# Performance work log

Hardware: AMD Instinct MI355X
Metric: run time of the kernel (lower is better)

## Reference

```python
import jax, jax.numpy as jnp
import numpy as np

T, IN_DIM, H1, H2 = 64, 84, 128, 84
BATCH = 8192


def _glorot(key, shape, fan):
    bound = 1.0 / np.sqrt(fan)
    return jax.random.uniform(key, shape, jnp.float32, -bound, bound)


def setup_inputs() -> dict:
    key = jax.random.key(0)
    ks = jax.random.split(key, 13)
    x = jax.random.normal(ks[0], (BATCH, T, IN_DIM, 1), jnp.float32)
    # rnn1 layer 0: 84 -> 128
    w_ih_l0 = _glorot(ks[1], (H1, IN_DIM), H1)
    w_hh_l0 = _glorot(ks[2], (H1, H1), H1)
    b_ih_l0 = _glorot(ks[3], (H1,), H1)
    b_hh_l0 = _glorot(ks[4], (H1,), H1)
    # rnn1 layer 1: 128 -> 128
    w_ih_l1 = _glorot(ks[5], (H1, H1), H1)
    w_hh_l1 = _glorot(ks[6], (H1, H1), H1)
    b_ih_l1 = _glorot(ks[7], (H1,), H1)
    b_hh_l1 = _glorot(ks[8], (H1,), H1)
    # rnn2: 128 -> 84
    w_ih_l2 = _glorot(ks[9], (H2, H1), H2)
    w_hh_l2 = _glorot(ks[10], (H2, H2), H2)
    b_ih_l2 = _glorot(ks[11], (H2,), H2)
    b_hh_l2 = _glorot(ks[12], (H2,), H2)
    return {
        "x": x,
        "w_ih_l0": w_ih_l0, "w_hh_l0": w_hh_l0, "b_ih_l0": b_ih_l0, "b_hh_l0": b_hh_l0,
        "w_ih_l1": w_ih_l1, "w_hh_l1": w_hh_l1, "b_ih_l1": b_ih_l1, "b_hh_l1": b_hh_l1,
        "w_ih_l2": w_ih_l2, "w_hh_l2": w_hh_l2, "b_ih_l2": b_ih_l2, "b_hh_l2": b_hh_l2,
    }


def _elman_layer(x, w_ih, w_hh, b_ih, b_hh):
    # x: (B, T, I) -> (B, T, H); h_t = tanh(x_t W_ih^T + b_ih + h_{t-1} W_hh^T + b_hh)
    # Precompute the input projection for all timesteps as one big GEMM.
    xp = jnp.einsum('bti,hi->bth', x, w_ih) + (b_ih + b_hh)  # (B, T, H)
    h0 = jnp.zeros((x.shape[0], w_hh.shape[0]), x.dtype)

    def step(h, xp_t):
        h = jnp.tanh(xp_t + h @ w_hh.T)
        return h, h

    _, ys = jax.lax.scan(step, h0, jnp.swapaxes(xp, 0, 1))  # (T, B, H)
    return jnp.swapaxes(ys, 0, 1)


def reference(x,
              w_ih_l0, w_hh_l0, b_ih_l0, b_hh_l0,
              w_ih_l1, w_hh_l1, b_ih_l1, b_hh_l1,
              w_ih_l2, w_hh_l2, b_ih_l2, b_hh_l2):
    x_ = jnp.squeeze(x, -1)                                   # (B, 64, 84)
    h = _elman_layer(x_, w_ih_l0, w_hh_l0, b_ih_l0, b_hh_l0)  # (B, 64, 128)
    h = _elman_layer(h, w_ih_l1, w_hh_l1, b_ih_l1, b_hh_l1)   # (B, 64, 128)
    h = _elman_layer(h, w_ih_l2, w_hh_l2, b_ih_l2, b_hh_l2)   # (B, 64, 84)
    return h[..., None]                                       # (B, 64, 84, 1)
```

## Files before the change

### kernel.cpp

```cpp
#include <hip/hip_runtime.h>


typedef __bf16 bf16x8 __attribute__((ext_vector_type(8)));
typedef float  f32x4  __attribute__((ext_vector_type(4)));
typedef float  f32x16 __attribute__((ext_vector_type(16)));
typedef unsigned short u16;
typedef unsigned int   u32;
typedef u16 u16x8 __attribute__((ext_vector_type(8)));
typedef u16 u16x4 __attribute__((ext_vector_type(4)));

#define MFMA32(a, b, c) __builtin_amdgcn_mfma_f32_32x32x16_bf16((a), (b), (c), 0, 0, 0)

__device__ __forceinline__ float bf2f(u16 v) {
    return __builtin_bit_cast(float, (u32)v << 16);
}
__device__ __forceinline__ u16 f2bf(float f) {
    u32 u = __builtin_bit_cast(u32, f);
    u = u + 0x7fffu + ((u >> 16) & 1u);
    return (u16)(u >> 16);
}
__device__ __forceinline__ float tanh_fast(float x) {
    float xc = fminf(fmaxf(x, -12.f), 12.f);
    float e  = __expf(2.f * xc);
    return (e - 1.f) * __builtin_amdgcn_rcpf(e + 1.f);
}
__device__ __forceinline__ bf16x8 ld_lds8(const u16* p) {
    return __builtin_bit_cast(bf16x8, *(const u16x8*)p);
}
__device__ __forceinline__ int aswz(int row, int off) {
    return row * 128 + (off ^ ((row & 7) << 3));
}
__device__ __forceinline__ void store4_hl(u16* ph, u16* pl, f32x4 v) {
    u16x4 hi, lo;
#pragma unroll
    for (int j = 0; j < 4; j++) {
        u16 h = f2bf(v[j]);
        hi[j] = h;
        lo[j] = f2bf(v[j] - bf2f(h));
    }
    *(u16x4*)ph = hi;
    *(u16x4*)pl = lo;
}

struct fragp { bf16x8 h, l; };

__device__ __forceinline__ fragp load_wfrag_hl(const float* W, int Hr, int Kr,
                                               int n, int kbase) {
    u16x8 uh = {0,0,0,0,0,0,0,0}, ul = {0,0,0,0,0,0,0,0};
    if (n < Hr) {
#pragma unroll
        for (int j = 0; j < 8; j++) {
            int k = kbase + j;
            if (k < Kr) {
                float w = W[n * Kr + k];
                u16 hi = f2bf(w);
                uh[j] = hi;
                ul[j] = f2bf(w - bf2f(hi));
            }
        }
    }
    fragp r;
    r.h = __builtin_bit_cast(bf16x8, uh);
    r.l = __builtin_bit_cast(bf16x8, ul);
    return r;
}

__device__ __forceinline__ f32x16 mm3t(const fragp& w, bf16x8 ah, bf16x8 al, f32x16 c) {
    c = MFMA32(w.h, ah, c);
    c = MFMA32(w.l, ah, c);
    c = MFMA32(w.h, al, c);
    return c;
}

#define STG_ISSUE(trr)                                                   \
    {                                                                    \
        const int tofs = (trr) * 84;                                     \
        _Pragma("unroll")                                                \
        for (int j = 0; j < 5; j++) xs[j] = xg[goff[j] + tofs];          \
        if (tid_s < 128) xs[5] = xg[goff[5] + tofs];                     \
    }
#define STG_WRITE(PNv)                                                   \
    {                                                                    \
        u16* bh = (&xbh[0][0][0]) + (PNv) * 3072;                        \
        u16* bl = (&xbl[0][0][0]) + (PNv) * 3072;                        \
        _Pragma("unroll")                                                \
        for (int j = 0; j < 5; j++) {                                    \
            u16 hi = f2bf(xs[j]);                                        \
            bh[lofs[j]] = hi;                                            \
            bl[lofs[j]] = f2bf(xs[j] - bf2f(hi));                        \
        }                                                                \
        if (tid_s < 128) {                                               \
            u16 hi = f2bf(xs[5]);                                        \
            bh[lofs[5]] = hi;                                            \
            bl[lofs[5]] = f2bf(xs[5] - bf2f(hi));                        \
        }                                                                \
    }

__global__ __launch_bounds__(768, 3)
void rnn_fused(const float* __restrict__ x,
               const float* __restrict__ wih0, const float* __restrict__ whh0,
               const float* __restrict__ bih0, const float* __restrict__ bhh0,
               const float* __restrict__ wih1, const float* __restrict__ whh1,
               const float* __restrict__ bih1, const float* __restrict__ bhh1,
               const float* __restrict__ wih2, const float* __restrict__ whh2,
               const float* __restrict__ bih2, const float* __restrict__ bhh2,
               float* __restrict__ out)
{
    __shared__ __align__(16) u16 h0h[2][4096], h0l[2][4096];
    __shared__ __align__(16) u16 h1h[2][4096], h1l[2][4096];
    __shared__ __align__(16) u16 h2h[2][4096], h2l[2][4096];
    __shared__ __align__(16) u16 xbh[2][32][96], xbl[2][32][96];
    __shared__ float biasF[3][128];

    const int tid  = threadIdx.x;
    const int wv   = tid >> 6;
    const int lane = tid & 63;
    const int mrow = lane & 31;
    const int q2   = lane >> 5;
    const int kq   = q2 * 8;
    const int q4   = q2 * 4;
    const int b0   = blockIdx.x * 32;
    const float* xg = x + (long)b0 * 5376;

    { u16* z = &h0h[0][0]; for (int i = tid; i < 4096; i += 768) z[i] = 0; }
    { u16* z = &h0l[0][0]; for (int i = tid; i < 4096; i += 768) z[i] = 0; }
    { u16* z = &h1h[1][0]; for (int i = tid; i < 4096; i += 768) z[i] = 0; }
    { u16* z = &h1l[1][0]; for (int i = tid; i < 4096; i += 768) z[i] = 0; }
    { u16* z = &h2h[0][0]; for (int i = tid; i < 4096; i += 768) z[i] = 0; }
    { u16* z = &h2l[0][0]; for (int i = tid; i < 4096; i += 768) z[i] = 0; }
    for (int i = tid; i < 32 * 12 * 2; i += 768) {
        int par = i / (32 * 12), rem = i - par * 32 * 12;
        int row = rem / 12, col = 84 + rem - row * 12;
        xbh[par][row][col] = 0; xbl[par][row][col] = 0;
    }
    for (int i = tid; i < 2688; i += 768) {
        int row = i / 84, col = i - row * 84;
        float v = xg[(long)row * 5376 + col];
        u16 hi = f2bf(v);
        xbh[0][row][col] = hi;
        xbl[0][row][col] = f2bf(v - bf2f(hi));
    }
    for (int i = tid; i < 384; i += 768) {
        int l = i >> 7, n = i & 127;
        float v = 0.f;
        if (l == 0)      v = bih0[n] + bhh0[n];
        else if (l == 1) v = bih1[n] + bhh1[n];
        else if (n < 84) v = bih2[n] + bhh2[n];
        biasF[l][n] = v;
    }
    __syncthreads();

    if (wv < 4) {
        const int nb = wv * 32;
        fragp fih0[6], fhh0[8];
#pragma unroll
        for (int c = 0; c < 6; c++)
            fih0[c] = load_wfrag_hl(wih0, 128, 84, nb + mrow, c * 16 + kq);
#pragma unroll
        for (int c = 0; c < 8; c++)
            fhh0[c] = load_wfrag_hl(whh0, 128, 128, nb + mrow, c * 16 + kq);
        const int tid_s = wv * 64 + lane;
        int goff[6], lofs[6];
#pragma unroll
        for (int j = 0; j < 6; j++) {
            int i = tid_s + j * 512, row = i / 84, cc = i - row * 84;
            goff[j] = row * 5376 + cc; lofs[j] = row * 96 + cc;
        }
        float xs[6];

        for (int rr = 0; rr < 66; ++rr) {
            const int P = rr & 1, PN = P ^ 1;
            if (rr <= 62) STG_ISSUE(rr + 1);
            if (rr <= 63) {
                f32x16 acc;
#pragma unroll
                for (int g = 0; g < 4; g++) {
                    f32x4 v = *(const f32x4*)&biasF[0][nb + g * 8 + q4];
                    acc[4*g+0] = v[0]; acc[4*g+1] = v[1];
                    acc[4*g+2] = v[2]; acc[4*g+3] = v[3];
                }
                __builtin_amdgcn_s_setprio(1);
#pragma unroll
                for (int c = 0; c < 6; c++) {
                    const int off = c * 16 + kq;
                    acc = mm3t(fih0[c], ld_lds8(&xbh[P][mrow][off]),
                                        ld_lds8(&xbl[P][mrow][off]), acc);
                }
#pragma unroll
                for (int c = 0; c < 8; c++) {
                    const int idx = aswz(mrow, c * 16 + kq);
                    acc = mm3t(fhh0[c], ld_lds8(&h0h[P][idx]), ld_lds8(&h0l[P][idx]), acc);
                }
                __builtin_amdgcn_s_setprio(0);
#pragma unroll
                for (int g = 0; g < 4; g++) {
                    const int col = nb + g * 8 + q4;
                    f32x4 v;
                    v[0] = tanh_fast(acc[4*g+0]); v[1] = tanh_fast(acc[4*g+1]);
                    v[2] = tanh_fast(acc[4*g+2]); v[3] = tanh_fast(acc[4*g+3]);
                    const int idx = mrow * 128 + (col ^ ((mrow & 7) << 3));
                    store4_hl(&h0h[PN][idx], &h0l[PN][idx], v);
                }
            }
            if (rr <= 62) STG_WRITE(PN);
            __syncthreads();
        }
    } else if (wv < 8) {
        const int nb = (wv - 4) * 32;
        fragp fih1[8], fhh1[8];
#pragma unroll
        for (int c = 0; c < 8; c++) {
            fih1[c] = load_wfrag_hl(wih1, 128, 128, nb + mrow, c * 16 + kq);
            fhh1[c] = load_wfrag_hl(whh1, 128, 128, nb + mrow, c * 16 + kq);
        }
        for (int rr = 0; rr < 66; ++rr) {
            const int P = rr & 1, PN = P ^ 1;
            if (rr >= 1 && rr <= 64) {
                f32x16 acc;
#pragma unroll
                for (int g = 0; g < 4; g++) {
                    f32x4 v = *(const f32x4*)&biasF[1][nb + g * 8 + q4];
                    acc[4*g+0] = v[0]; acc[4*g+1] = v[1];
                    acc[4*g+2] = v[2]; acc[4*g+3] = v[3];
                }
                __builtin_amdgcn_s_setprio(1);
#pragma unroll
                for (int c = 0; c < 8; c++) {
                    const int idx = aswz(mrow, c * 16 + kq);
                    acc = mm3t(fih1[c], ld_lds8(&h0h[P][idx]), ld_lds8(&h0l[P][idx]), acc);
                }
#pragma unroll
                for (int c = 0; c < 8; c++) {
                    const int idx = aswz(mrow, c * 16 + kq);
                    acc = mm3t(fhh1[c], ld_lds8(&h1h[P][idx]), ld_lds8(&h1l[P][idx]), acc);
                }
                __builtin_amdgcn_s_setprio(0);
#pragma unroll
                for (int g = 0; g < 4; g++) {
                    const int col = nb + g * 8 + q4;
                    f32x4 v;
                    v[0] = tanh_fast(acc[4*g+0]); v[1] = tanh_fast(acc[4*g+1]);
                    v[2] = tanh_fast(acc[4*g+2]); v[3] = tanh_fast(acc[4*g+3]);
                    const int idx = mrow * 128 + (col ^ ((mrow & 7) << 3));
                    store4_hl(&h1h[PN][idx], &h1l[PN][idx], v);
                }
            }
            __syncthreads();
        }
    } else if (wv < 11) {
        const int nb = (wv - 8) * 32;
        fragp fih2[8], fhh2[6];
#pragma unroll
        for (int c = 0; c < 8; c++)
            fih2[c] = load_wfrag_hl(wih2, 84, 128, nb + mrow, c * 16 + kq);
#pragma unroll
        for (int c = 0; c < 6; c++)
            fhh2[c] = load_wfrag_hl(whh2, 84, 84, nb + mrow, c * 16 + kq);
        const int tid_s = (wv - 4) * 64 + lane;
        int goff[6], lofs[6];
#pragma unroll
        for (int j = 0; j < 6; j++) {
            int i = tid_s + j * 512, row = i / 84, cc = i - row * 84;
            goff[j] = row * 5376 + cc; lofs[j] = row * 96 + cc;
        }
        float xs[6];

        for (int rr = 0; rr < 66; ++rr) {
            const int P = rr & 1, PN = P ^ 1;
            if (rr <= 62) STG_ISSUE(rr + 1);
            if (rr >= 2) {
                const int t2 = rr - 2;
                f32x16 acc;
#pragma unroll
                for (int g = 0; g < 4; g++) {
                    f32x4 v = *(const f32x4*)&biasF[2][nb + g * 8 + q4];
                    acc[4*g+0] = v[0]; acc[4*g+1] = v[1];
                    acc[4*g+2] = v[2]; acc[4*g+3] = v[3];
                }
                __builtin_amdgcn_s_setprio(1);
#pragma unroll
                for (int c = 0; c < 8; c++) {
                    const int idx = aswz(mrow, c * 16 + kq);
                    acc = mm3t(fih2[c], ld_lds8(&h1h[P][idx]), ld_lds8(&h1l[P][idx]), acc);
                }
#pragma unroll
                for (int c = 0; c < 6; c++) {
                    const int idx = aswz(mrow, c * 16 + kq);
                    acc = mm3t(fhh2[c], ld_lds8(&h2h[P][idx]), ld_lds8(&h2l[P][idx]), acc);
                }
                __builtin_amdgcn_s_setprio(0);
#pragma unroll
                for (int g = 0; g < 4; g++) {
                    const int col = nb + g * 8 + q4;
                    f32x4 v;
                    v[0] = tanh_fast(acc[4*g+0]); v[1] = tanh_fast(acc[4*g+1]);
                    v[2] = tanh_fast(acc[4*g+2]); v[3] = tanh_fast(acc[4*g+3]);
                    const int idx = mrow * 128 + (col ^ ((mrow & 7) << 3));
                    store4_hl(&h2h[PN][idx], &h2l[PN][idx], v);
                    if (col < 84)
                        *(f32x4*)(out + (long)(b0 + mrow) * 5376 + t2 * 84 + col) = v;
                }
            }
            if (rr <= 62) STG_WRITE(PN);
            __syncthreads();
        }
    } else {
        const int tid_s = 7 * 64 + lane;
        int goff[6], lofs[6];
#pragma unroll
        for (int j = 0; j < 6; j++) {
            int i = tid_s + j * 512, row = i / 84, cc = i - row * 84;
            goff[j] = row * 5376 + cc; lofs[j] = row * 96 + cc;
        }
        float xs[6];
        for (int rr = 0; rr < 66; ++rr) {
            const int PN = (rr & 1) ^ 1;
            if (rr <= 62) STG_ISSUE(rr + 1);
            if (rr <= 62) STG_WRITE(PN);
            __syncthreads();
        }
    }
}

extern "C" void kernel_launch(void* const* d_in, const int* in_sizes, int n_in,
                              void* d_out, int out_size, void* d_ws, size_t ws_size,
                              hipStream_t stream) {
    (void)in_sizes; (void)n_in; (void)out_size; (void)d_ws; (void)ws_size;
    const float* x    = (const float*)d_in[0];
    const float* wih0 = (const float*)d_in[1];
    const float* whh0 = (const float*)d_in[2];
    const float* bih0 = (const float*)d_in[3];
    const float* bhh0 = (const float*)d_in[4];
    const float* wih1 = (const float*)d_in[5];
    const float* whh1 = (const float*)d_in[6];
    const float* bih1 = (const float*)d_in[7];
    const float* bhh1 = (const float*)d_in[8];
    const float* wih2 = (const float*)d_in[9];
    const float* whh2 = (const float*)d_in[10];
    const float* bih2 = (const float*)d_in[11];
    const float* bhh2 = (const float*)d_in[12];
    float* out = (float*)d_out;

    rnn_fused<<<dim3(8192 / 32), dim3(768), 0, stream>>>(
        x, wih0, whh0, bih0, bhh0, wih1, whh1, bih1, bhh1,
        wih2, whh2, bih2, bhh2, out);
}
```

Before: 555.5 us.

## Split MFMA accumulator chains and vectorize swizzled x staging

Each layer's recurrent MFMA chain now alternates between two independent accumulators that are summed before tanh. This shortens the dependent MFMA chain so back-to-back MFMAs can overlap. The x input staging switches from scalar float loads and u16 LDS stores to float4 global loads and vectorized hi/lo stores into a 128-wide swizzled LDS buffer, which also makes x reads use the same aswz indexing as hidden states. The cost is more LDS for the x buffers, extra accumulator registers, and one extra vector add per step.

New measurement: 592.6 us. 1.07x slower.

```diff
diff --git a/kernel.cpp b/kernel.cpp
--- a/kernel.cpp
+++ b/kernel.cpp
@@ -75,26 +75,27 @@
 #define STG_ISSUE(trr)                                                   \
     {                                                                    \
         const int tofs = (trr) * 84;                                     \
-        _Pragma("unroll")                                                \
-        for (int j = 0; j < 5; j++) xs[j] = xg[goff[j] + tofs];          \
-        if (tid_s < 128) xs[5] = xg[goff[5] + tofs];                     \
+        xq0 = *(const f32x4*)&xg[goffq0 + tofs];                         \
+        if (tid_s < 160) xq1 = *(const f32x4*)&xg[goffq1 + tofs];        \
     }
 #define STG_WRITE(PNv)                                                   \
     {                                                                    \
-        u16* bh = (&xbh[0][0][0]) + (PNv) * 3072;                        \
-        u16* bl = (&xbl[0][0][0]) + (PNv) * 3072;                        \
-        _Pragma("unroll")                                                \
-        for (int j = 0; j < 5; j++) {                                    \
-            u16 hi = f2bf(xs[j]);                                        \
-            bh[lofs[j]] = hi;                                            \
-            bl[lofs[j]] = f2bf(xs[j] - bf2f(hi));                        \
-        }                                                                \
-        if (tid_s < 128) {                                               \
-            u16 hi = f2bf(xs[5]);                                        \
-            bh[lofs[5]] = hi;                                            \
-            bl[lofs[5]] = f2bf(xs[5] - bf2f(hi));                        \
-        }                                                                \
-    }
+        u16* bh = &xbh[(PNv)][0];                                        \
+        u16* bl = &xbl[(PNv)][0];                                        \
+        store4_hl(&bh[lofsq0], &bl[lofsq0], xq0);                        \
+        if (tid_s < 160) store4_hl(&bh[lofsq1], &bl[lofsq1], xq1);       \
+    }
+#define STG_SETUP()                                                      \
+    int goffq0, lofsq0, goffq1, lofsq1;                                  \
+    {                                                                    \
+        int r0 = tid_s / 21, c0 = (tid_s - r0 * 21) * 4;                 \
+        goffq0 = r0 * 5376 + c0;                                         \
+        lofsq0 = r0 * 128 + (c0 ^ ((r0 & 7) << 3));                      \
+        int s1 = tid_s + 512, r1 = s1 / 21, c1 = (s1 - r1 * 21) * 4;     \
+        goffq1 = r1 * 5376 + c1;                                         \
+        lofsq1 = r1 * 128 + (c1 ^ ((r1 & 7) << 3));                      \
+    }                                                                    \
+    f32x4 xq0, xq1;
 
 __global__ __launch_bounds__(768, 3)
 void rnn_fused(const float* __restrict__ x,
@@ -109,7 +110,7 @@
     __shared__ __align__(16) u16 h0h[2][4096], h0l[2][4096];
     __shared__ __align__(16) u16 h1h[2][4096], h1l[2][4096];
     __shared__ __align__(16) u16 h2h[2][4096], h2l[2][4096];
-    __shared__ __align__(16) u16 xbh[2][32][96], xbl[2][32][96];
+    __shared__ __align__(16) u16 xbh[2][4096], xbl[2][4096];
     __shared__ float biasF[3][128];
 
     const int tid  = threadIdx.x;
@@ -128,17 +129,13 @@
     { u16* z = &h1l[1][0]; for (int i = tid; i < 4096; i += 768) z[i] = 0; }
     { u16* z = &h2h[0][0]; for (int i = tid; i < 4096; i += 768) z[i] = 0; }
     { u16* z = &h2l[0][0]; for (int i = tid; i < 4096; i += 768) z[i] = 0; }
-    for (int i = tid; i < 32 * 12 * 2; i += 768) {
-        int par = i / (32 * 12), rem = i - par * 32 * 12;
-        int row = rem / 12, col = 84 + rem - row * 12;
-        xbh[par][row][col] = 0; xbl[par][row][col] = 0;
-    }
-    for (int i = tid; i < 2688; i += 768) {
-        int row = i / 84, col = i - row * 84;
-        float v = xg[(long)row * 5376 + col];
-        u16 hi = f2bf(v);
-        xbh[0][row][col] = hi;
-        xbl[0][row][col] = f2bf(v - bf2f(hi));
+    { u16* z = &xbh[0][0]; for (int i = tid; i < 8192; i += 768) z[i] = 0; }
+    { u16* z = &xbl[0][0]; for (int i = tid; i < 8192; i += 768) z[i] = 0; }
+    for (int s = tid; s < 672; s += 768) {
+        int row = s / 21, cq = (s - row * 21) * 4;
+        f32x4 v = *(const f32x4*)&xg[(long)row * 5376 + cq];
+        int idx = row * 128 + (cq ^ ((row & 7) << 3));
+        store4_hl(&xbh[0][idx], &xbl[0][idx], v);
     }
     for (int i = tid; i < 384; i += 768) {
         int l = i >> 7, n = i & 127;
@@ -160,38 +157,38 @@
         for (int c = 0; c < 8; c++)
             fhh0[c] = load_wfrag_hl(whh0, 128, 128, nb + mrow, c * 16 + kq);
         const int tid_s = wv * 64 + lane;
-        int goff[6], lofs[6];
-#pragma unroll
-        for (int j = 0; j < 6; j++) {
-            int i = tid_s + j * 512, row = i / 84, cc = i - row * 84;
-            goff[j] = row * 5376 + cc; lofs[j] = row * 96 + cc;
-        }
-        float xs[6];
+        STG_SETUP();
 
         for (int rr = 0; rr < 66; ++rr) {
             const int P = rr & 1, PN = P ^ 1;
             if (rr <= 62) STG_ISSUE(rr + 1);
             if (rr <= 63) {
-                f32x16 acc;
+                f32x16 accA, accB;
 #pragma unroll
                 for (int g = 0; g < 4; g++) {
                     f32x4 v = *(const f32x4*)&biasF[0][nb + g * 8 + q4];
-                    acc[4*g+0] = v[0]; acc[4*g+1] = v[1];
-                    acc[4*g+2] = v[2]; acc[4*g+3] = v[3];
-                }
+                    accA[4*g+0] = v[0]; accA[4*g+1] = v[1];
+                    accA[4*g+2] = v[2]; accA[4*g+3] = v[3];
+                }
+#pragma unroll
+                for (int i = 0; i < 16; i++) accB[i] = 0.f;
                 __builtin_amdgcn_s_setprio(1);
 #pragma unroll
                 for (int c = 0; c < 6; c++) {
-                    const int off = c * 16 + kq;
-                    acc = mm3t(fih0[c], ld_lds8(&xbh[P][mrow][off]),
-                                        ld_lds8(&xbl[P][mrow][off]), acc);
+                    const int idx = aswz(mrow, c * 16 + kq);
+                    bf16x8 ah = ld_lds8(&xbh[P][idx]), al = ld_lds8(&xbl[P][idx]);
+                    if (c & 1) accA = mm3t(fih0[c], ah, al, accA);
+                    else       accB = mm3t(fih0[c], ah, al, accB);
                 }
 #pragma unroll
                 for (int c = 0; c < 8; c++) {
                     const int idx = aswz(mrow, c * 16 + kq);
-                    acc = mm3t(fhh0[c], ld_lds8(&h0h[P][idx]), ld_lds8(&h0l[P][idx]), acc);
+                    bf16x8 ah = ld_lds8(&h0h[P][idx]), al = ld_lds8(&h0l[P][idx]);
+                    if (c & 1) accA = mm3t(fhh0[c], ah, al, accA);
+                    else       accB = mm3t(fhh0[c], ah, al, accB);
                 }
                 __builtin_amdgcn_s_setprio(0);
+                f32x16 acc = accA + accB;
 #pragma unroll
                 for (int g = 0; g < 4; g++) {
                     const int col = nb + g * 8 + q4;
@@ -216,25 +213,32 @@
         for (int rr = 0; rr < 66; ++rr) {
             const int P = rr & 1, PN = P ^ 1;
             if (rr >= 1 && rr <= 64) {
-                f32x16 acc;
+                f32x16 accA, accB;
 #pragma unroll
                 for (int g = 0; g < 4; g++) {
                     f32x4 v = *(const f32x4*)&biasF[1][nb + g * 8 + q4];
-                    acc[4*g+0] = v[0]; acc[4*g+1] = v[1];
-                    acc[4*g+2] = v[2]; acc[4*g+3] = v[3];
-                }
+                    accA[4*g+0] = v[0]; accA[4*g+1] = v[1];
+                    accA[4*g+2] = v[2]; accA[4*g+3] = v[3];
+                }
+#pragma unroll
+                for (int i = 0; i < 16; i++) accB[i] = 0.f;
                 __builtin_amdgcn_s_setprio(1);
 #pragma unroll
                 for (int c = 0; c < 8; c++) {
                     const int idx = aswz(mrow, c * 16 + kq);
-                    acc = mm3t(fih1[c], ld_lds8(&h0h[P][idx]), ld_lds8(&h0l[P][idx]), acc);
+                    bf16x8 ah = ld_lds8(&h0h[P][idx]), al = ld_lds8(&h0l[P][idx]);
+                    if (c & 1) accA = mm3t(fih1[c], ah, al, accA);
+                    else       accB = mm3t(fih1[c], ah, al, accB);
                 }
 #pragma unroll
                 for (int c = 0; c < 8; c++) {
                     const int idx = aswz(mrow, c * 16 + kq);
-                    acc = mm3t(fhh1[c], ld_lds8(&h1h[P][idx]), ld_lds8(&h1l[P][idx]), acc);
+                    bf16x8 ah = ld_lds8(&h1h[P][idx]), al = ld_lds8(&h1l[P][idx]);
+                    if (c & 1) accA = mm3t(fhh1[c], ah, al, accA);
+                    else       accB = mm3t(fhh1[c], ah, al, accB);
                 }
                 __builtin_amdgcn_s_setprio(0);
+                f32x16 acc = accA + accB;
 #pragma unroll
                 for (int g = 0; g < 4; g++) {
                     const int col = nb + g * 8 + q4;
@@ -257,38 +261,39 @@
         for (int c = 0; c < 6; c++)
             fhh2[c] = load_wfrag_hl(whh2, 84, 84, nb + mrow, c * 16 + kq);
         const int tid_s = (wv - 4) * 64 + lane;
-        int goff[6], lofs[6];
-#pragma unroll
-        for (int j = 0; j < 6; j++) {
-            int i = tid_s + j * 512, row = i / 84, cc = i - row * 84;
-            goff[j] = row * 5376 + cc; lofs[j] = row * 96 + cc;
-        }
-        float xs[6];
+        STG_SETUP();
 
         for (int rr = 0; rr < 66; ++rr) {
             const int P = rr & 1, PN = P ^ 1;
             if (rr <= 62) STG_ISSUE(rr + 1);
             if (rr >= 2) {
                 const int t2 = rr - 2;
-                f32x16 acc;
+                f32x16 accA, accB;
 #pragma unroll
                 for (int g = 0; g < 4; g++) {
                     f32x4 v = *(const f32x4*)&biasF[2][nb + g * 8 + q4];
-                    acc[4*g+0] = v[0]; acc[4*g+1] = v[1];
-                    acc[4*g+2] = v[2]; acc[4*g+3] = v[3];
-                }
+                    accA[4*g+0] = v[0]; accA[4*g+1] = v[1];
+                    accA[4*g+2] = v[2]; accA[4*g+3] = v[3];
+                }
+#pragma unroll
+                for (int i = 0; i < 16; i++) accB[i] = 0.f;
                 __builtin_amdgcn_s_setprio(1);
 #pragma unroll
                 for (int c = 0; c < 8; c++) {
                     const int idx = aswz(mrow, c * 16 + kq);
-                    acc = mm3t(fih2[c], ld_lds8(&h1h[P][idx]), ld_lds8(&h1l[P][idx]), acc);
+                    bf16x8 ah = ld_lds8(&h1h[P][idx]), al = ld_lds8(&h1l[P][idx]);
+                    if (c & 1) accA = mm3t(fih2[c], ah, al, accA);
+                    else       accB = mm3t(fih2[c], ah, al, accB);
                 }
 #pragma unroll
                 for (int c = 0; c < 6; c++) {
                     const int idx = aswz(mrow, c * 16 + kq);
-                    acc = mm3t(fhh2[c], ld_lds8(&h2h[P][idx]), ld_lds8(&h2l[P][idx]), acc);
+                    bf16x8 ah = ld_lds8(&h2h[P][idx]), al = ld_lds8(&h2l[P][idx]);
+                    if (c & 1) accA = mm3t(fhh2[c], ah, al, accA);
+                    else       accB = mm3t(fhh2[c], ah, al, accB);
                 }
                 __builtin_amdgcn_s_setprio(0);
+                f32x16 acc = accA + accB;
 #pragma unroll
                 for (int g = 0; g < 4; g++) {
                     const int col = nb + g * 8 + q4;
@@ -306,13 +311,7 @@
         }
     } else {
         const int tid_s = 7 * 64 + lane;
-        int goff[6], lofs[6];
-#pragma unroll
-        for (int j = 0; j < 6; j++) {
-            int i = tid_s + j * 512, row = i / 84, cc = i - row * 84;
-            goff[j] = row * 5376 + cc; lofs[j] = row * 96 + cc;
-        }
-        float xs[6];
+        STG_SETUP();
         for (int rr = 0; rr < 66; ++rr) {
             const int PN = (rr & 1) ^ 1;
             if (rr <= 62) STG_ISSUE(rr + 1);
```
